# Kernel tuning notes

Hardware: AMD Instinct MI355X
Metric: run time of the kernel (lower is better)

Reference implementation:

```python
import jax, jax.numpy as jnp
import numpy as np

K = 3          # pooling factor (init k)
H_OUT = 8      # number of bilinear heads
H_DIM = 512    # hidden dim after pooling
BN_EPS = 1e-5
NEG_INF = -jnp.inf


def setup_inputs() -> dict:
    key = jax.random.key(0)
    ks = jax.random.split(key, 8)
    b, vn, qn, vd, qd = 16, 256, 256, 512, 768
    hk = H_DIM * K
    return {
        "v": jax.random.normal(ks[0], (b, vn, vd), jnp.float32),
        "q": jax.random.normal(ks[1], (b, qn, qd), jnp.float32),
        "Wv": jax.random.normal(ks[2], (hk, vd), jnp.float32) * 0.05,
        "bv": jax.random.normal(ks[3], (hk,), jnp.float32) * 0.05,
        "Wq": jax.random.normal(ks[4], (hk, qd), jnp.float32) * 0.05,
        "bq": jax.random.normal(ks[5], (hk,), jnp.float32) * 0.05,
        "h_mat": jax.random.normal(ks[6], (1, H_OUT, 1, hk), jnp.float32),
        "h_bias": jax.random.normal(ks[7], (1, H_OUT, 1, 1), jnp.float32),
        "bn_gamma": jnp.ones((H_DIM,), jnp.float32),
        "bn_beta": jnp.zeros((H_DIM,), jnp.float32),
    }


def _forward(v, q, Wv, bv, Wq, bq, h_mat, h_bias, bn_gamma, bn_beta):
    # FCNet (eval mode: dropout is identity; weight_norm folded into W)
    v_ = jax.nn.relu(jnp.einsum("bvd,kd->bvk", v, Wv) + bv)   # [b, vn, h_dim*k]
    q_ = jax.nn.relu(jnp.einsum("bqd,kd->bqk", q, Wq) + bq)   # [b, qn, h_dim*k]

    # Bilinear attention maps: [b, h_out, vn, qn]
    att = jnp.einsum("xhyk,bvk,bqk->bhvq", h_mat, v_, q_) + h_bias

    # v_mask / q_mask (all-zero token rows masked to -inf)
    v_zero = jnp.sum(jnp.abs(v), axis=2) == 0                  # [b, vn]
    q_zero = jnp.sum(jnp.abs(q), axis=2) == 0                  # [b, qn]
    att = jnp.where(v_zero[:, None, :, None], NEG_INF, att)
    att = jnp.where(q_zero[:, None, None, :], NEG_INF, att)

    # Fused per-head attention pooling, summed over heads (original Python loop)
    fused = jnp.einsum("bhvq,bqk->bhvk", att, q_)
    logits_k = jnp.einsum("bvk,bhvk->bk", v_, fused)           # [b, h_dim*k]

    # AvgPool1d(k, stride=k) * k  == sum over groups of k
    b = logits_k.shape[0]
    logits = logits_k.reshape(b, H_DIM, K).sum(axis=2)         # [b, h_dim]

    # BatchNorm1d (training-mode batch statistics, biased variance)
    mu = logits.mean(axis=0)
    var = logits.var(axis=0)
    logits = (logits - mu) * jax.lax.rsqrt(var + BN_EPS) * bn_gamma + bn_beta
    return logits, att


def reference(v, q, Wv, bv, Wq, bq, h_mat, h_bias, bn_gamma, bn_beta):
    return _forward(v, q, Wv, bv, Wq, bq, h_mat, h_bias, bn_gamma, bn_beta)
```

## Files before the change

kernel.cpp:

```cpp
#include <hip/hip_runtime.h>
#include <math.h>

#define BB    16
#define VN    256
#define QN    256
#define VD    512
#define QD    768
#define HK    1536
#define HDIM  512

typedef _Float16 half8 __attribute__((ext_vector_type(8)));
typedef _Float16 half4 __attribute__((ext_vector_type(4)));
typedef float f32x4 __attribute__((ext_vector_type(4)));

__global__ __launch_bounds__(256) void conv_mask2(
    const float* __restrict__ v, const float* __restrict__ q,
    _Float16* __restrict__ v16, _Float16* __restrict__ q16,
    float* __restrict__ vz, float* __restrict__ qz) {
    int which = blockIdx.y;
    const float* src = which ? q : v;
    _Float16* dst = which ? q16 : v16;
    float* outz = which ? qz : vz;
    int D = which ? QD : VD;
    int w = threadIdx.x >> 6, ln = threadIdx.x & 63;
    int row = blockIdx.x * 4 + w;
    const float* p = src + (size_t)row * D;
    _Float16* d = dst + (size_t)row * D;
    float s = 0.f;
    for (int c = ln * 4; c < D; c += 256) {
        float4 x = *(const float4*)(p + c);
        s += fabsf(x.x) + fabsf(x.y) + fabsf(x.z) + fabsf(x.w);
        half4 hh = {(_Float16)x.x, (_Float16)x.y, (_Float16)x.z, (_Float16)x.w};
        *(half4*)(d + c) = hh;
    }
    for (int off = 32; off > 0; off >>= 1) s += __shfl_down(s, off);
    if (ln == 0) outz[row] = (s == 0.f) ? 1.f : 0.f;
}

__global__ __launch_bounds__(256) void conv_w3(
    const float* __restrict__ Wv, _Float16* __restrict__ Wv16, int n4v,
    const float* __restrict__ Wq, _Float16* __restrict__ Wq16, int n4q,
    const float* __restrict__ hm, _Float16* __restrict__ hs16) {
    if (blockIdx.y == 2) {
        int k = blockIdx.x * 256 + threadIdx.x;
        if (k >= HK) return;
        float s = 0.f;
#pragma unroll
        for (int h = 0; h < 8; ++h) {
            float x = hm[h * HK + k];
            s += x;
            hs16[h * HK + k] = (_Float16)x;
        }
        hs16[8 * HK + k] = (_Float16)s;
        return;
    }
    const float* src = blockIdx.y ? Wq : Wv;
    _Float16* dst = blockIdx.y ? Wq16 : Wv16;
    int n4 = blockIdx.y ? n4q : n4v;
    int i = blockIdx.x * 256 + threadIdx.x;
    if (i < n4) {
        float4 x = ((const float4*)src)[i];
        half4 h = {(_Float16)x.x, (_Float16)x.y, (_Float16)x.z, (_Float16)x.w};
        ((half4*)dst)[i] = h;
    }
}

__global__ __launch_bounds__(256, 2) void proj128(
    const _Float16* __restrict__ v16in, const _Float16* __restrict__ Wv16,
    const float* __restrict__ bv, _Float16* __restrict__ v16,
    const _Float16* __restrict__ q16in, const _Float16* __restrict__ Wq16,
    const float* __restrict__ bq, _Float16* __restrict__ q16) {
    __shared__ _Float16 As[128 * 64];
    __shared__ _Float16 Bs[128 * 64];
    int z = blockIdx.z;
    const _Float16* Ain = z ? q16in : v16in;
    const _Float16* W16 = z ? Wq16 : Wv16;
    const float* bias = z ? bq : bv;
    _Float16* C16 = z ? q16 : v16;
    int K = z ? QD : VD;
    int m0 = blockIdx.y * 128, n0 = blockIdx.x * 128;
    int t = threadIdx.x;
    int w = t >> 6, ln = t & 63, quad = ln >> 4, r16 = ln & 15;
    int wi = w & 1, wj = w >> 1;
    int arow = t >> 3, aseg = t & 7;
    int sg = (aseg ^ (arow & 7)) * 8;
    const _Float16* ApG = Ain + (size_t)(m0 + arow) * K + aseg * 8;
    const _Float16* BpG = W16 + (size_t)(n0 + arow) * K + aseg * 8;
    half8 ra[4], rb[4];
#pragma unroll
    for (int c = 0; c < 4; ++c) {
        ra[c] = *(const half8*)(ApG + (size_t)c * 32 * K);
        rb[c] = *(const half8*)(BpG + (size_t)c * 32 * K);
    }
    f32x4 acc[4][4] = {};
    for (int k0 = 0; k0 < K; k0 += 64) {
        __syncthreads();
#pragma unroll
        for (int c = 0; c < 4; ++c) {
            *(half8*)&As[(c * 32 + arow) * 64 + sg] = ra[c];
            *(half8*)&Bs[(c * 32 + arow) * 64 + sg] = rb[c];
        }
        __syncthreads();
        if (k0 + 64 < K) {
#pragma unroll
            for (int c = 0; c < 4; ++c) {
                ra[c] = *(const half8*)(ApG + (size_t)c * 32 * K + k0 + 64);
                rb[c] = *(const half8*)(BpG + (size_t)c * 32 * K + k0 + 64);
            }
        }
#pragma unroll
        for (int kc = 0; kc < 2; ++kc) {
            half8 af[4], bf[4];
#pragma unroll
            for (int fi = 0; fi < 4; ++fi) {
                int rl = wi * 64 + fi * 16 + r16;
                af[fi] = *(const half8*)&As[rl * 64 + ((kc * 4 + quad) ^ (rl & 7)) * 8];
            }
#pragma unroll
            for (int fj = 0; fj < 4; ++fj) {
                int rl = wj * 64 + fj * 16 + r16;
                bf[fj] = *(const half8*)&Bs[rl * 64 + ((kc * 4 + quad) ^ (rl & 7)) * 8];
            }
#pragma unroll
            for (int fi = 0; fi < 4; ++fi)
#pragma unroll
                for (int fj = 0; fj < 4; ++fj)
                    acc[fi][fj] = __builtin_amdgcn_mfma_f32_16x16x32_f16(
                        af[fi], bf[fj], acc[fi][fj], 0, 0, 0);
        }
    }
#pragma unroll
    for (int fi = 0; fi < 4; ++fi) {
#pragma unroll
        for (int r = 0; r < 4; ++r) {
            int m = m0 + wi * 64 + fi * 16 + quad * 4 + r;
#pragma unroll
            for (int fj = 0; fj < 4; ++fj) {
                int n = n0 + wj * 64 + fj * 16 + r16;
                float x = acc[fi][fj][r] + bias[n];
                C16[(size_t)m * HK + n] = (_Float16)fmaxf(x, 0.f);
            }
        }
    }
}

__global__ __launch_bounds__(256, 2) void att_db(
    const _Float16* __restrict__ v16, const _Float16* __restrict__ q16,
    const _Float16* __restrict__ hs16, const float* __restrict__ hb,
    const float* __restrict__ vz, const float* __restrict__ qz,
    float* __restrict__ att_out, _Float16* __restrict__ A16) {
    __shared__ _Float16 As[2][64 * 64];
    __shared__ _Float16 Bs[2][32 * 64];
    __shared__ _Float16 Hl[8 * HK];
    int lin = blockIdx.x;
    int swz = ((lin & 7) << 6) | (lin >> 3);
    int jb = swz & 7, ib = (swz >> 3) & 3, b = swz >> 5;
    int i0 = ib * 64, j0 = jb * 32;
    int t = threadIdx.x;
    int w = t >> 6, ln = t & 63, quad = ln >> 4, r16 = ln & 15;
    int iw = w & 1, hg = w >> 1, h0 = hg * 4;
    int arow = t >> 3, aseg = t & 7;
    int sg = (aseg ^ (arow & 7)) * 8;
    for (int u = t * 8; u < 8 * HK; u += 256 * 8)
        *(half8*)&Hl[u] = *(const half8*)(hs16 + u);
    const _Float16* ApG = v16 + (size_t)b * VN * HK + (size_t)(i0 + arow) * HK + aseg * 8;
    const _Float16* BpG = q16 + (size_t)b * QN * HK + (size_t)(j0 + arow) * HK + aseg * 8;
    half8 ra[2], rb;
    ra[0] = *(const half8*)(ApG);
    ra[1] = *(const half8*)(ApG + (size_t)32 * HK);
    rb    = *(const half8*)(BpG);
    *(half8*)&As[0][arow * 64 + sg] = ra[0];
    *(half8*)&As[0][(arow + 32) * 64 + sg] = ra[1];
    *(half8*)&Bs[0][arow * 64 + sg] = rb;
    ra[0] = *(const half8*)(ApG + 64);
    ra[1] = *(const half8*)(ApG + (size_t)32 * HK + 64);
    rb    = *(const half8*)(BpG + 64);
    f32x4 acc[4][2][2] = {};
    for (int it = 0; it < 24; ++it) {
        __syncthreads();
        int cur = it & 1;
        const _Float16* Ac = As[cur];
        const _Float16* Bc = Bs[cur];
        if (it + 1 < 24) {
            int nxt = cur ^ 1;
            *(half8*)&As[nxt][arow * 64 + sg] = ra[0];
            *(half8*)&As[nxt][(arow + 32) * 64 + sg] = ra[1];
            *(half8*)&Bs[nxt][arow * 64 + sg] = rb;
        }
        if (it + 2 < 24) {
            int kn = (it + 2) * 64;
            ra[0] = *(const half8*)(ApG + kn);
            ra[1] = *(const half8*)(ApG + (size_t)32 * HK + kn);
            rb    = *(const half8*)(BpG + kn);
        }
        int kb = it * 64;
#pragma unroll
        for (int kc = 0; kc < 2; ++kc) {
            half8 af[2], bf[2];
#pragma unroll
            for (int fi = 0; fi < 2; ++fi) {
                int rl = iw * 32 + fi * 16 + r16;
                af[fi] = *(const half8*)&Ac[rl * 64 + ((kc * 4 + quad) ^ (rl & 7)) * 8];
            }
#pragma unroll
            for (int fj = 0; fj < 2; ++fj) {
                int rl = fj * 16 + r16;
                bf[fj] = *(const half8*)&Bc[rl * 64 + ((kc * 4 + quad) ^ (rl & 7)) * 8];
            }
#pragma unroll
            for (int hh = 0; hh < 4; ++hh) {
                half8 hmv = *(const half8*)&Hl[(h0 + hh) * HK + kb + (kc * 4 + quad) * 8];
#pragma unroll
                for (int fi = 0; fi < 2; ++fi) {
                    half8 am = af[fi] * hmv;
#pragma unroll
                    for (int fj = 0; fj < 2; ++fj)
                        acc[hh][fi][fj] = __builtin_amdgcn_mfma_f32_16x16x32_f16(
                            am, bf[fj], acc[hh][fi][fj], 0, 0, 0);
                }
            }
        }
    }
    float s[2][2][4];
#pragma unroll
    for (int fi = 0; fi < 2; ++fi)
#pragma unroll
        for (int fj = 0; fj < 2; ++fj)
#pragma unroll
            for (int r = 0; r < 4; ++r) {
                float ss = 0.f;
#pragma unroll
                for (int hh = 0; hh < 4; ++hh) ss += acc[hh][fi][fj][r];
                s[fi][fj][r] = ss;
            }
    float hbv[4];
#pragma unroll
    for (int hh = 0; hh < 4; ++hh) hbv[hh] = hb[h0 + hh];
    float hbsum = 0.f;
#pragma unroll
    for (int h = 0; h < 8; ++h) hbsum += hb[h];
    float qm[2];
#pragma unroll
    for (int fj = 0; fj < 2; ++fj) qm[fj] = qz[b * QN + j0 + fj * 16 + r16];
    float* outb = att_out + (size_t)b * 8 * VN * QN;
#pragma unroll
    for (int fi = 0; fi < 2; ++fi) {
#pragma unroll
        for (int r = 0; r < 4; ++r) {
            int i = i0 + iw * 32 + fi * 16 + quad * 4 + r;
            float vm = vz[b * VN + i];
#pragma unroll
            for (int fj = 0; fj < 2; ++fj) {
                int j = j0 + fj * 16 + r16;
                bool msk = (vm != 0.f) || (qm[fj] != 0.f);
#pragma unroll
                for (int hh = 0; hh < 4; ++hh) {
                    float x = acc[hh][fi][fj][r] + hbv[hh];
                    if (msk) x = -INFINITY;
                    outb[(size_t)(h0 + hh) * VN * QN + (size_t)i * QN + j] = x;
                }
            }
        }
    }
    __syncthreads();
    float* Red = (float*)&As[0][0];
    if (hg) {
#pragma unroll
        for (int fi = 0; fi < 2; ++fi)
#pragma unroll
            for (int fj = 0; fj < 2; ++fj)
#pragma unroll
                for (int r = 0; r < 4; ++r)
                    Red[iw * 1024 + (fi * 16 + quad * 4 + r) * 32 + fj * 16 + r16] =
                        s[fi][fj][r];
    }
    __syncthreads();
    if (!hg) {
        _Float16* Ab = A16 + (size_t)b * VN * QN;
#pragma unroll
        for (int fi = 0; fi < 2; ++fi) {
#pragma unroll
            for (int r = 0; r < 4; ++r) {
                int i = i0 + iw * 32 + fi * 16 + quad * 4 + r;
                float vm = vz[b * VN + i];
#pragma unroll
                for (int fj = 0; fj < 2; ++fj) {
                    int j = j0 + fj * 16 + r16;
                    float tot = s[fi][fj][r] +
                                Red[iw * 1024 + (fi * 16 + quad * 4 + r) * 32 + fj * 16 + r16] +
                                hbsum;
                    if (vm != 0.f || qm[fj] != 0.f) tot = -INFINITY;
                    Ab[(size_t)i * QN + j] = (_Float16)tot;
                }
            }
        }
    }
}

__global__ __launch_bounds__(256) void transpose_q16(const _Float16* __restrict__ q16,
                                                     _Float16* __restrict__ q16t) {
    __shared__ _Float16 Ls[32][72];
    int b = blockIdx.z;
    int k0 = blockIdx.x * 64, j0 = blockIdx.y * 32;
    int t = threadIdx.x;
    const _Float16* src = q16 + (size_t)b * QN * HK;
    int tj = t >> 3, tk = (t & 7) * 8;
    half8 vv = *(const half8*)(src + (size_t)(j0 + tj) * HK + k0 + tk);
#pragma unroll
    for (int e = 0; e < 8; ++e) Ls[tj][tk + e] = vv[e];
    __syncthreads();
    int ok = t >> 2, oj = (t & 3) * 8;
    half8 ov;
#pragma unroll
    for (int e = 0; e < 8; ++e) ov[e] = Ls[oj + e][ok];
    *(half8*)(q16t + (size_t)b * HK * QN + (size_t)(k0 + ok) * QN + j0 + oj) = ov;
}

__global__ __launch_bounds__(256) void t_lk_mfma(
    const _Float16* __restrict__ A16, const _Float16* __restrict__ q16t,
    const _Float16* __restrict__ v16, float* __restrict__ lk) {
    __shared__ _Float16 As[256 * 32];
    __shared__ _Float16 Bs[64 * 32];
    __shared__ float red[16][64];
    int b = blockIdx.y;
    int k0 = blockIdx.x * 64;
    int t = threadIdx.x;
    int w = t >> 6, ln = t & 63, quad = ln >> 4, r16 = ln & 15;
    const _Float16* Ab = A16 + (size_t)b * VN * QN;
    const _Float16* Qt = q16t + (size_t)b * HK * QN + (size_t)k0 * QN;
    int ar = t >> 2, aseg = t & 3;
    f32x4 acc[4][4] = {};
    for (int j0 = 0; j0 < QN; j0 += 32) {
        half8 a0 = *(const half8*)(Ab + (size_t)(ar +   0) * QN + j0 + aseg * 8);
        half8 a1 = *(const half8*)(Ab + (size_t)(ar +  64) * QN + j0 + aseg * 8);
        half8 a2 = *(const half8*)(Ab + (size_t)(ar + 128) * QN + j0 + aseg * 8);
        half8 a3 = *(const half8*)(Ab + (size_t)(ar + 192) * QN + j0 + aseg * 8);
        half8 bv = *(const half8*)(Qt + (size_t)ar * QN + j0 + aseg * 8);
        __syncthreads();
        *(half8*)&As[(ar +   0) * 32 + aseg * 8] = a0;
        *(half8*)&As[(ar +  64) * 32 + aseg * 8] = a1;
        *(half8*)&As[(ar + 128) * 32 + aseg * 8] = a2;
        *(half8*)&As[(ar + 192) * 32 + aseg * 8] = a3;
        *(half8*)&Bs[ar * 32 + aseg * 8] = bv;
        __syncthreads();
        half8 af[4], bf[4];
#pragma unroll
        for (int fi = 0; fi < 4; ++fi)
            af[fi] = *(const half8*)&As[(w * 64 + fi * 16 + r16) * 32 + quad * 8];
#pragma unroll
        for (int fj = 0; fj < 4; ++fj)
            bf[fj] = *(const half8*)&Bs[(fj * 16 + r16) * 32 + quad * 8];
#pragma unroll
        for (int fi = 0; fi < 4; ++fi)
#pragma unroll
            for (int fj = 0; fj < 4; ++fj)
                acc[fi][fj] = __builtin_amdgcn_mfma_f32_16x16x32_f16(
                    af[fi], bf[fj], acc[fi][fj], 0, 0, 0);
    }
    const _Float16* Vb = v16 + (size_t)b * VN * HK;
    float part[4] = {0.f, 0.f, 0.f, 0.f};
#pragma unroll
    for (int fi = 0; fi < 4; ++fi) {
#pragma unroll
        for (int r = 0; r < 4; ++r) {
            int i = w * 64 + fi * 16 + quad * 4 + r;
#pragma unroll
            for (int fj = 0; fj < 4; ++fj) {
                float vv = (float)Vb[(size_t)i * HK + k0 + fj * 16 + r16];
                part[fj] += acc[fi][fj][r] * vv;
            }
        }
    }
#pragma unroll
    for (int fj = 0; fj < 4; ++fj)
        red[w * 4 + quad][fj * 16 + r16] = part[fj];
    __syncthreads();
    if (t < 64) {
        float s = 0.f;
#pragma unroll
        for (int g = 0; g < 16; ++g) s += red[g][t];
        lk[b * HK + k0 + t] = s;
    }
}

__global__ __launch_bounds__(256) void bn_kernel(
    const float* __restrict__ lk, const float* __restrict__ gamma,
    const float* __restrict__ beta, float* __restrict__ out) {
    int d = blockIdx.x * blockDim.x + threadIdx.x;
    if (d >= HDIM) return;
    float l[BB];
    float mu = 0.f;
#pragma unroll
    for (int b = 0; b < BB; ++b) {
        const float* p = lk + b * HK + 3 * d;
        float s = p[0] + p[1] + p[2];
        l[b] = s;
        mu += s;
    }
    mu *= (1.f / BB);
    float var = 0.f;
#pragma unroll
    for (int b = 0; b < BB; ++b) {
        float dd = l[b] - mu;
        var += dd * dd;
    }
    var *= (1.f / BB);
    float inv = rsqrtf(var + 1e-5f);
    float g = gamma[d], be = beta[d];
#pragma unroll
    for (int b = 0; b < BB; ++b)
        out[b * HDIM + d] = (l[b] - mu) * inv * g + be;
}

extern "C" void kernel_launch(void* const* d_in, const int* in_sizes, int n_in,
                              void* d_out, int out_size, void* d_ws, size_t ws_size,
                              hipStream_t stream) {
    const float* v  = (const float*)d_in[0];
    const float* q  = (const float*)d_in[1];
    const float* Wv = (const float*)d_in[2];
    const float* bv = (const float*)d_in[3];
    const float* Wq = (const float*)d_in[4];
    const float* bq = (const float*)d_in[5];
    const float* hm = (const float*)d_in[6];
    const float* hb = (const float*)d_in[7];
    const float* gamma = (const float*)d_in[8];
    const float* beta  = (const float*)d_in[9];

    float* out_logits = (float*)d_out;
    float* out_att    = out_logits + BB * HDIM;

    _Float16* h = (_Float16*)d_ws;
    _Float16* v16   = h;
    _Float16* q16   = v16 + (size_t)BB * VN * HK;
    _Float16* q16t  = q16 + (size_t)BB * QN * HK;
    _Float16* A16   = q16t + (size_t)BB * HK * QN;
    _Float16* v16in = A16 + (size_t)BB * VN * QN;
    _Float16* q16in = v16in + (size_t)BB * VN * VD;
    _Float16* Wv16  = q16in + (size_t)BB * QN * QD;
    _Float16* Wq16  = Wv16 + (size_t)HK * VD;
    _Float16* hs16  = Wq16 + (size_t)HK * QD;
    float* lk = (float*)(hs16 + 9 * HK + 8);
    float* vz = lk + BB * HK;
    float* qz = vz + BB * VN;

    conv_mask2<<<dim3(BB * VN / 4, 2), 256, 0, stream>>>(v, q, v16in, q16in, vz, qz);
    conv_w3<<<dim3((HK * QD / 4 + 255) / 256, 3), 256, 0, stream>>>(
        Wv, Wv16, HK * VD / 4, Wq, Wq16, HK * QD / 4, hm, hs16);

    proj128<<<dim3(HK / 128, BB * VN / 128, 2), 256, 0, stream>>>(
        v16in, Wv16, bv, v16, q16in, Wq16, bq, q16);

    att_db<<<dim3(512), 256, 0, stream>>>(
        v16, q16, hs16, hb, vz, qz, out_att, A16);

    transpose_q16<<<dim3(HK / 64, QN / 32, BB), 256, 0, stream>>>(q16, q16t);

    t_lk_mfma<<<dim3(HK / 64, BB), 256, 0, stream>>>(A16, q16t, v16, lk);

    bn_kernel<<<dim3((HDIM + 255) / 256), 256, 0, stream>>>(lk, gamma, beta, out_logits);
}
```

Baseline: 179.2 us.

## Fuse fp32-to-fp16 conversion and zero-row mask into projection GEMM loads

```diff
diff --git a/kernel.cpp b/kernel.cpp
--- a/kernel.cpp
+++ b/kernel.cpp
@@ -13,84 +13,68 @@
 typedef _Float16 half4 __attribute__((ext_vector_type(4)));
 typedef float f32x4 __attribute__((ext_vector_type(4)));
 
-__global__ __launch_bounds__(256) void conv_mask2(
+__device__ inline half8 ld_cvt8(const float* p) {
+    float4 a = *(const float4*)p;
+    float4 b = *(const float4*)(p + 4);
+    half8 h = {(_Float16)a.x, (_Float16)a.y, (_Float16)a.z, (_Float16)a.w,
+               (_Float16)b.x, (_Float16)b.y, (_Float16)b.z, (_Float16)b.w};
+    return h;
+}
+__device__ inline half8 ld_cvt8_abs(const float* p, float& s) {
+    float4 a = *(const float4*)p;
+    float4 b = *(const float4*)(p + 4);
+    s += fabsf(a.x) + fabsf(a.y) + fabsf(a.z) + fabsf(a.w) +
+         fabsf(b.x) + fabsf(b.y) + fabsf(b.z) + fabsf(b.w);
+    half8 h = {(_Float16)a.x, (_Float16)a.y, (_Float16)a.z, (_Float16)a.w,
+               (_Float16)b.x, (_Float16)b.y, (_Float16)b.z, (_Float16)b.w};
+    return h;
+}
+
+__global__ __launch_bounds__(256) void conv_hm(
+    const float* __restrict__ hm, _Float16* __restrict__ hs16) {
+    int k = blockIdx.x * 256 + threadIdx.x;
+    if (k >= HK) return;
+    float s = 0.f;
+#pragma unroll
+    for (int h = 0; h < 8; ++h) {
+        float x = hm[h * HK + k];
+        s += x;
+        hs16[h * HK + k] = (_Float16)x;
+    }
+    hs16[8 * HK + k] = (_Float16)s;
+}
+
+__global__ __launch_bounds__(256, 2) void proj128m(
     const float* __restrict__ v, const float* __restrict__ q,
+    const float* __restrict__ Wv, const float* __restrict__ Wq,
+    const float* __restrict__ bv, const float* __restrict__ bq,
     _Float16* __restrict__ v16, _Float16* __restrict__ q16,
     float* __restrict__ vz, float* __restrict__ qz) {
-    int which = blockIdx.y;
-    const float* src = which ? q : v;
-    _Float16* dst = which ? q16 : v16;
-    float* outz = which ? qz : vz;
-    int D = which ? QD : VD;
-    int w = threadIdx.x >> 6, ln = threadIdx.x & 63;
-    int row = blockIdx.x * 4 + w;
-    const float* p = src + (size_t)row * D;
-    _Float16* d = dst + (size_t)row * D;
-    float s = 0.f;
-    for (int c = ln * 4; c < D; c += 256) {
-        float4 x = *(const float4*)(p + c);
-        s += fabsf(x.x) + fabsf(x.y) + fabsf(x.z) + fabsf(x.w);
-        half4 hh = {(_Float16)x.x, (_Float16)x.y, (_Float16)x.z, (_Float16)x.w};
-        *(half4*)(d + c) = hh;
-    }
-    for (int off = 32; off > 0; off >>= 1) s += __shfl_down(s, off);
-    if (ln == 0) outz[row] = (s == 0.f) ? 1.f : 0.f;
-}
-
-__global__ __launch_bounds__(256) void conv_w3(
-    const float* __restrict__ Wv, _Float16* __restrict__ Wv16, int n4v,
-    const float* __restrict__ Wq, _Float16* __restrict__ Wq16, int n4q,
-    const float* __restrict__ hm, _Float16* __restrict__ hs16) {
-    if (blockIdx.y == 2) {
-        int k = blockIdx.x * 256 + threadIdx.x;
-        if (k >= HK) return;
-        float s = 0.f;
-#pragma unroll
-        for (int h = 0; h < 8; ++h) {
-            float x = hm[h * HK + k];
-            s += x;
-            hs16[h * HK + k] = (_Float16)x;
-        }
-        hs16[8 * HK + k] = (_Float16)s;
-        return;
-    }
-    const float* src = blockIdx.y ? Wq : Wv;
-    _Float16* dst = blockIdx.y ? Wq16 : Wv16;
-    int n4 = blockIdx.y ? n4q : n4v;
-    int i = blockIdx.x * 256 + threadIdx.x;
-    if (i < n4) {
-        float4 x = ((const float4*)src)[i];
-        half4 h = {(_Float16)x.x, (_Float16)x.y, (_Float16)x.z, (_Float16)x.w};
-        ((half4*)dst)[i] = h;
-    }
-}
-
-__global__ __launch_bounds__(256, 2) void proj128(
-    const _Float16* __restrict__ v16in, const _Float16* __restrict__ Wv16,
-    const float* __restrict__ bv, _Float16* __restrict__ v16,
-    const _Float16* __restrict__ q16in, const _Float16* __restrict__ Wq16,
-    const float* __restrict__ bq, _Float16* __restrict__ q16) {
     __shared__ _Float16 As[128 * 64];
     __shared__ _Float16 Bs[128 * 64];
     int z = blockIdx.z;
-    const _Float16* Ain = z ? q16in : v16in;
-    const _Float16* W16 = z ? Wq16 : Wv16;
+    const float* Ain = z ? q : v;
+    const float* Wf  = z ? Wq : Wv;
     const float* bias = z ? bq : bv;
     _Float16* C16 = z ? q16 : v16;
+    float* outz = z ? qz : vz;
     int K = z ? QD : VD;
     int m0 = blockIdx.y * 128, n0 = blockIdx.x * 128;
+    bool domask = (blockIdx.x == 0);
     int t = threadIdx.x;
     int w = t >> 6, ln = t & 63, quad = ln >> 4, r16 = ln & 15;
     int wi = w & 1, wj = w >> 1;
     int arow = t >> 3, aseg = t & 7;
     int sg = (aseg ^ (arow & 7)) * 8;
-    const _Float16* ApG = Ain + (size_t)(m0 + arow) * K + aseg * 8;
-    const _Float16* BpG = W16 + (size_t)(n0 + arow) * K + aseg * 8;
+    const float* ApG = Ain + (size_t)(m0 + arow) * K + aseg * 8;
+    const float* BpG = Wf + (size_t)(n0 + arow) * K + aseg * 8;
+    float sabs[4] = {0.f, 0.f, 0.f, 0.f};
     half8 ra[4], rb[4];
 #pragma unroll
     for (int c = 0; c < 4; ++c) {
-        ra[c] = *(const half8*)(ApG + (size_t)c * 32 * K);
-        rb[c] = *(const half8*)(BpG + (size_t)c * 32 * K);
+        if (domask) ra[c] = ld_cvt8_abs(ApG + (size_t)c * 32 * K, sabs[c]);
+        else        ra[c] = ld_cvt8(ApG + (size_t)c * 32 * K);
+        rb[c] = ld_cvt8(BpG + (size_t)c * 32 * K);
     }
     f32x4 acc[4][4] = {};
     for (int k0 = 0; k0 < K; k0 += 64) {
@@ -104,8 +88,9 @@
         if (k0 + 64 < K) {
 #pragma unroll
             for (int c = 0; c < 4; ++c) {
-                ra[c] = *(const half8*)(ApG + (size_t)c * 32 * K + k0 + 64);
-                rb[c] = *(const half8*)(BpG + (size_t)c * 32 * K + k0 + 64);
+                if (domask) ra[c] = ld_cvt8_abs(ApG + (size_t)c * 32 * K + k0 + 64, sabs[c]);
+                else        ra[c] = ld_cvt8(ApG + (size_t)c * 32 * K + k0 + 64);
+                rb[c] = ld_cvt8(BpG + (size_t)c * 32 * K + k0 + 64);
             }
         }
 #pragma unroll
@@ -127,6 +112,16 @@
                 for (int fj = 0; fj < 4; ++fj)
                     acc[fi][fj] = __builtin_amdgcn_mfma_f32_16x16x32_f16(
                         af[fi], bf[fj], acc[fi][fj], 0, 0, 0);
+        }
+    }
+    if (domask) {
+#pragma unroll
+        for (int c = 0; c < 4; ++c) {
+            float s = sabs[c];
+            s += __shfl_down(s, 4);
+            s += __shfl_down(s, 2);
+            s += __shfl_down(s, 1);
+            if (aseg == 0) outz[m0 + c * 32 + arow] = (s == 0.f) ? 1.f : 0.f;
         }
     }
 #pragma unroll
@@ -434,21 +429,15 @@
     _Float16* q16   = v16 + (size_t)BB * VN * HK;
     _Float16* q16t  = q16 + (size_t)BB * QN * HK;
     _Float16* A16   = q16t + (size_t)BB * HK * QN;
-    _Float16* v16in = A16 + (size_t)BB * VN * QN;
-    _Float16* q16in = v16in + (size_t)BB * VN * VD;
-    _Float16* Wv16  = q16in + (size_t)BB * QN * QD;
-    _Float16* Wq16  = Wv16 + (size_t)HK * VD;
-    _Float16* hs16  = Wq16 + (size_t)HK * QD;
+    _Float16* hs16  = A16 + (size_t)BB * VN * QN;
     float* lk = (float*)(hs16 + 9 * HK + 8);
     float* vz = lk + BB * HK;
     float* qz = vz + BB * VN;
 
-    conv_mask2<<<dim3(BB * VN / 4, 2), 256, 0, stream>>>(v, q, v16in, q16in, vz, qz);
-    conv_w3<<<dim3((HK * QD / 4 + 255) / 256, 3), 256, 0, stream>>>(
-        Wv, Wv16, HK * VD / 4, Wq, Wq16, HK * QD / 4, hm, hs16);
-
-    proj128<<<dim3(HK / 128, BB * VN / 128, 2), 256, 0, stream>>>(
-        v16in, Wv16, bv, v16, q16in, Wq16, bq, q16);
+    conv_hm<<<dim3((HK + 255) / 256), 256, 0, stream>>>(hm, hs16);
+
+    proj128m<<<dim3(HK / 128, BB * VN / 128, 2), 256, 0, stream>>>(
+        v, q, Wv, Wq, bv, bq, v16, q16, vz, qz);
 
     att_db<<<dim3(512), 256, 0, stream>>>(
         v16, q16, hs16, hb, vz, qz, out_att, A16);
```

Result: slower. 196.2 us (+9.5%).
